# Kernel optimization log

Measured on AMD Instinct MI355X. Metric: run time of the kernel, lower is better.

Reference implementation:

```python
import jax, jax.numpy as jnp
import numpy as np

DIM_INPUT = 100000
DIM_LATENT = 128
NNZ = 819200
BATCH = 16384


def setup_inputs() -> dict:
    key = jax.random.key(0)
    k1, k2, k3, k4, k5 = jax.random.split(key, 5)
    vals = jax.random.uniform(k1, (NNZ,), dtype=jnp.float32)
    row_idx = jnp.sort(jax.random.randint(k2, (NNZ,), 0, BATCH, dtype=jnp.int32))
    col_idx = jax.random.randint(k3, (NNZ,), 0, DIM_INPUT, dtype=jnp.int32)
    # learned parameters (match torch init: w0 zeros, w/v randn)
    w0 = jnp.zeros((1,), dtype=jnp.float32)
    w = jax.random.normal(k4, (DIM_INPUT,), dtype=jnp.float32)
    v = jax.random.normal(k5, (DIM_INPUT, DIM_LATENT), dtype=jnp.float32)
    return {"vals": vals, "row_idx": row_idx, "col_idx": col_idx,
            "batch": BATCH, "w0": w0, "w": w, "v": v}


def reference(vals, row_idx, col_idx, batch, w0, w, v):
    # x is a sparse [batch, dim_input] matrix in COO form (row_idx, col_idx, vals).
    # linear term: w0 + x @ w
    linear = w0[0] + jax.ops.segment_sum(vals * w[col_idx], row_idx,
                                         num_segments=batch)
    # gather latent rows once: [nnz, K]
    v_rows = v[col_idx]
    weighted = vals[:, None] * v_rows                      # [nnz, K]
    xv = jax.ops.segment_sum(weighted, row_idx, num_segments=batch)       # [B, K]
    x_v_sq = jax.ops.segment_sum(weighted * v_rows, row_idx,
                                 num_segments=batch)       # x @ (v**2): [B, K]
    interaction = 0.5 * (jnp.sum(xv * xv, axis=1) - jnp.sum(x_v_sq, axis=1))
    return linear + interaction
```

## Files before the change

### kernel.cpp

```cpp
#include <hip/hip_runtime.h>

#define FM_NNZ   819200
#define FM_BATCH 16384
#define FM_DIM   100000
#define FM_K     128
#define NB_SHIFT 13
#define NBUCK    13
#define BAD_COL  (1 << 20)


static __device__ __forceinline__ uint32_t f2bf(float f) {
    uint32_t u = __float_as_uint(f);
    return (u + 0x7fffu + ((u >> 16) & 1u)) >> 16;
}

__global__ __launch_bounds__(256) void cvt_kernel(const float* __restrict__ v,
                                                  uint32_t* __restrict__ vb) {
    const float4* __restrict__ v4 = (const float4*)v;
    uint2* __restrict__ o = (uint2*)vb;
    const int n = (FM_DIM * FM_K) / 4;
    for (int i = blockIdx.x * blockDim.x + threadIdx.x; i < n;
         i += gridDim.x * blockDim.x) {
        const float4 x = v4[i];
        uint2 r;
        r.x = f2bf(x.x) | (f2bf(x.y) << 16);
        r.y = f2bf(x.z) | (f2bf(x.w) << 16);
        o[i] = r;
    }
}


__global__ __launch_bounds__(256, 8) void fm_fwd_kernel(
    const float* __restrict__ vals,
    const int*   __restrict__ row_idx,
    const int*   __restrict__ col_idx,
    const float* __restrict__ w0,
    const float* __restrict__ w_,
    const uint32_t* __restrict__ vb,
    float*       __restrict__ out)
{
    const int wave = threadIdx.x >> 6;
    const int lane = threadIdx.x & 63;
    const int wid  = blockIdx.x * 4 + wave;
    const int row0 = 2 * wid;
    const int row1 = row0 + 1;

    int s[3];
    #pragma unroll
    for (int q = 0; q < 3; ++q) {
        const int key = row0 + q;
        int lo = 0, hi = FM_NNZ;
        while (lo < hi) {
            const int mid = (lo + hi) >> 1;
            if (row_idx[mid] < key) lo = mid + 1; else hi = mid;
        }
        s[q] = lo;
    }
    const int s0 = s[0], s1 = s[1], s2 = s[2];

    int   cA, cB, cC, cD;
    float aA, aB, aC, aD;
    {
        int idx, ic; bool ok;
        idx = s0 + lane;      ok = idx < s1; ic = min(idx, FM_NNZ - 1);
        cA = ok ? col_idx[ic] : BAD_COL;  aA = ok ? vals[ic] : 0.f;
        idx = s0 + 64 + lane; ok = idx < s1; ic = min(idx, FM_NNZ - 1);
        cB = ok ? col_idx[ic] : BAD_COL;  aB = ok ? vals[ic] : 0.f;
        idx = s1 + lane;      ok = idx < s2; ic = min(idx, FM_NNZ - 1);
        cC = ok ? col_idx[ic] : BAD_COL;  aC = ok ? vals[ic] : 0.f;
        idx = s1 + 64 + lane; ok = idx < s2; ic = min(idx, FM_NNZ - 1);
        cD = ok ? col_idx[ic] : BAD_COL;  aD = ok ? vals[ic] : 0.f;
    }

    float xv0l = 0.f, xv0h = 0.f, sq0l = 0.f, sq0h = 0.f, lin0 = 0.f;
    float xv1l = 0.f, xv1h = 0.f, sq1l = 0.f, sq1h = 0.f, lin1 = 0.f;

#define WALK(creg, areg, xlo, xhi, slo, shi, linr)                         \
    {                                                                      \
        unsigned long long m = __ballot(((creg) >> NB_SHIFT) == p);        \
        while (m) {                                                        \
            const int j = __ffsll((unsigned long long)m) - 1;              \
            m &= m - 1;                                                    \
            const int   cj = __shfl((creg), j);                            \
            const float aj = __shfl((areg), j);                            \
            const uint32_t u = vb[(size_t)cj * 64 + lane];                 \
            linr = fmaf(aj, w_[cj], linr);             \
            const float vlo = __uint_as_float(u << 16);                    \
            const float vhi = __uint_as_float(u & 0xffff0000u);            \
            const float tl = aj * vlo, th = aj * vhi;                      \
            xlo += tl;  xhi += th;                                         \
            slo = fmaf(tl, vlo, slo);  shi = fmaf(th, vhi, shi);           \
        }                                                                  \
    }

    for (int p = 0; p < NBUCK; ++p) {
        WALK(cA, aA, xv0l, xv0h, sq0l, sq0h, lin0)
        WALK(cB, aB, xv0l, xv0h, sq0l, sq0h, lin0)
        WALK(cC, aC, xv1l, xv1h, sq1l, sq1h, lin1)
        WALK(cD, aD, xv1l, xv1h, sq1l, sq1h, lin1)
    }
#undef WALK

    float part0 = xv0l * xv0l + xv0h * xv0h - sq0l - sq0h;
    float part1 = xv1l * xv1l + xv1h * xv1h - sq1l - sq1h;
    #pragma unroll
    for (int off = 32; off > 0; off >>= 1) {
        part0 += __shfl_down(part0, off);
        part1 += __shfl_down(part1, off);
    }
    if (lane == 0) {
        const float bias = w0[0];
        out[row0] = bias + lin0 + 0.5f * part0;
        out[row1] = bias + lin1 + 0.5f * part1;
    }
}

extern "C" void kernel_launch(void* const* d_in, const int* in_sizes, int n_in,
                              void* d_out, int out_size, void* d_ws, size_t ws_size,
                              hipStream_t stream) {
    const float* vals    = (const float*)d_in[0];
    const int*   row_idx = (const int*)  d_in[1];
    const int*   col_idx = (const int*)  d_in[2];
    const float* w0      = (const float*)d_in[4];
    const float* w       = (const float*)d_in[5];
    const float* v       = (const float*)d_in[6];
    float*       out     = (float*)d_out;
    uint32_t*    vb      = (uint32_t*)d_ws;

    cvt_kernel<<<1024, 256, 0, stream>>>(v, vb);
    fm_fwd_kernel<<<FM_BATCH / 8, 256, 0, stream>>>(
        vals, row_idx, col_idx, w0, w, vb, out);
}
```

Before: 174.7 us.

## Compact bucket-sorted nonzeros into LDS and batch gathers eight at a time

```diff
diff --git a/kernel.cpp b/kernel.cpp
--- a/kernel.cpp
+++ b/kernel.cpp
@@ -6,7 +6,7 @@
 #define FM_K     128
 #define NB_SHIFT 13
 #define NBUCK    13
-#define BAD_COL  (1 << 20)
+#define GBATCH   8
 
 
 static __device__ __forceinline__ uint32_t f2bf(float f) {
@@ -39,11 +39,12 @@
     const uint32_t* __restrict__ vb,
     float*       __restrict__ out)
 {
+    __shared__ uint2 lists[4][2][128];
+
     const int wave = threadIdx.x >> 6;
     const int lane = threadIdx.x & 63;
     const int wid  = blockIdx.x * 4 + wave;
     const int row0 = 2 * wid;
-    const int row1 = row0 + 1;
 
     int s[3];
     #pragma unroll
@@ -58,48 +59,84 @@
     }
     const int s0 = s[0], s1 = s[1], s2 = s[2];
 
-    int   cA, cB, cC, cD;
-    float aA, aB, aC, aD;
+    int cA, cB, cC, cD;  float aA, aB, aC, aD;  int bA, bB, bC, bD;
     {
         int idx, ic; bool ok;
         idx = s0 + lane;      ok = idx < s1; ic = min(idx, FM_NNZ - 1);
-        cA = ok ? col_idx[ic] : BAD_COL;  aA = ok ? vals[ic] : 0.f;
+        cA = col_idx[ic]; aA = ok ? vals[ic] : 0.f; bA = ok ? (cA >> NB_SHIFT) : 127;
         idx = s0 + 64 + lane; ok = idx < s1; ic = min(idx, FM_NNZ - 1);
-        cB = ok ? col_idx[ic] : BAD_COL;  aB = ok ? vals[ic] : 0.f;
+        cB = col_idx[ic]; aB = ok ? vals[ic] : 0.f; bB = ok ? (cB >> NB_SHIFT) : 127;
         idx = s1 + lane;      ok = idx < s2; ic = min(idx, FM_NNZ - 1);
-        cC = ok ? col_idx[ic] : BAD_COL;  aC = ok ? vals[ic] : 0.f;
+        cC = col_idx[ic]; aC = ok ? vals[ic] : 0.f; bC = ok ? (cC >> NB_SHIFT) : 127;
         idx = s1 + 64 + lane; ok = idx < s2; ic = min(idx, FM_NNZ - 1);
-        cD = ok ? col_idx[ic] : BAD_COL;  aD = ok ? vals[ic] : 0.f;
+        cD = col_idx[ic]; aD = ok ? vals[ic] : 0.f; bD = ok ? (cD >> NB_SHIFT) : 127;
     }
 
-    float xv0l = 0.f, xv0h = 0.f, sq0l = 0.f, sq0h = 0.f, lin0 = 0.f;
-    float xv1l = 0.f, xv1h = 0.f, sq1l = 0.f, sq1h = 0.f, lin1 = 0.f;
+    float lin0 = aA * w_[cA] + aB * w_[cB];
+    float lin1 = aC * w_[cC] + aD * w_[cD];
 
-#define WALK(creg, areg, xlo, xhi, slo, shi, linr)                         \
-    {                                                                      \
-        unsigned long long m = __ballot(((creg) >> NB_SHIFT) == p);        \
-        while (m) {                                                        \
-            const int j = __ffsll((unsigned long long)m) - 1;              \
-            m &= m - 1;                                                    \
-            const int   cj = __shfl((creg), j);                            \
-            const float aj = __shfl((areg), j);                            \
-            const uint32_t u = vb[(size_t)cj * 64 + lane];                 \
-            linr = fmaf(aj, w_[cj], linr);             \
-            const float vlo = __uint_as_float(u << 16);                    \
-            const float vhi = __uint_as_float(u & 0xffff0000u);            \
-            const float tl = aj * vlo, th = aj * vhi;                      \
-            xlo += tl;  xhi += th;                                         \
-            slo = fmaf(tl, vlo, slo);  shi = fmaf(th, vhi, shi);           \
-        }                                                                  \
+    const unsigned long long lt = (1ull << lane) - 1ull;
+    int total0, total1;
+    {
+        int posA = -1, posB = -1, run = 0;
+        for (int p = 0; p < NBUCK; ++p) {
+            const unsigned long long mA = __ballot(bA == p);
+            const unsigned long long mB = __ballot(bB == p);
+            const int nA = __popcll(mA);
+            if (bA == p) posA = run + __popcll(mA & lt);
+            if (bB == p) posB = run + nA + __popcll(mB & lt);
+            run += nA + __popcll(mB);
+        }
+        total0 = run;
+        if (posA >= 0) lists[wave][0][posA] = make_uint2((uint32_t)cA, __float_as_uint(aA));
+        if (posB >= 0) lists[wave][0][posB] = make_uint2((uint32_t)cB, __float_as_uint(aB));
+    }
+    {
+        int posC = -1, posD = -1, run = 0;
+        for (int p = 0; p < NBUCK; ++p) {
+            const unsigned long long mC = __ballot(bC == p);
+            const unsigned long long mD = __ballot(bD == p);
+            const int nC = __popcll(mC);
+            if (bC == p) posC = run + __popcll(mC & lt);
+            if (bD == p) posD = run + nC + __popcll(mD & lt);
+            run += nC + __popcll(mD);
+        }
+        total1 = run;
+        if (posC >= 0) lists[wave][1][posC] = make_uint2((uint32_t)cC, __float_as_uint(aC));
+        if (posD >= 0) lists[wave][1][posD] = make_uint2((uint32_t)cD, __float_as_uint(aD));
+    }
+    __syncthreads();
+
+    float xv0l = 0.f, xv0h = 0.f, sq0l = 0.f, sq0h = 0.f;
+    float xv1l = 0.f, xv1h = 0.f, sq1l = 0.f, sq1h = 0.f;
+
+#define ROWWALK(r, total, xvl, xvh, sql, sqh)                                 \
+    for (int i = 0; i < (total); i += GBATCH) {                               \
+        uint2    ca[GBATCH];                                                  \
+        uint32_t vv[GBATCH];                                                  \
+        _Pragma("unroll")                                                     \
+        for (int u = 0; u < GBATCH; ++u) {                                    \
+            const int e = min(i + u, (total) - 1);                            \
+            ca[u] = lists[wave][r][e];             \
+        }                                                                     \
+        _Pragma("unroll")                                                     \
+        for (int u = 0; u < GBATCH; ++u) {                                    \
+            vv[u] = vb[(size_t)ca[u].x * 64 + lane];  \
+        }                                                                     \
+        _Pragma("unroll")                                                     \
+        for (int u = 0; u < GBATCH; ++u) {                                    \
+            const float aj  = (i + u < (total)) ? __uint_as_float(ca[u].y) : 0.f; \
+            const float vlo = __uint_as_float(vv[u] << 16);                   \
+            const float vhi = __uint_as_float(vv[u] & 0xffff0000u);           \
+            const float tl = aj * vlo, th = aj * vhi;                         \
+            xvl += tl;  xvh += th;                                            \
+            sql = fmaf(tl, vlo, sql);  sqh = fmaf(th, vhi, sqh);              \
+        }                                                                     \
     }
 
-    for (int p = 0; p < NBUCK; ++p) {
-        WALK(cA, aA, xv0l, xv0h, sq0l, sq0h, lin0)
-        WALK(cB, aB, xv0l, xv0h, sq0l, sq0h, lin0)
-        WALK(cC, aC, xv1l, xv1h, sq1l, sq1h, lin1)
-        WALK(cD, aD, xv1l, xv1h, sq1l, sq1h, lin1)
-    }
-#undef WALK
+    ROWWALK(0, total0, xv0l, xv0h, sq0l, sq0h)
+    ROWWALK(1, total1, xv1l, xv1h, sq1l, sq1h)
+#undef ROWWALK
 
     float part0 = xv0l * xv0l + xv0h * xv0h - sq0l - sq0h;
     float part1 = xv1l * xv1l + xv1h * xv1h - sq1l - sq1h;
@@ -107,11 +144,13 @@
     for (int off = 32; off > 0; off >>= 1) {
         part0 += __shfl_down(part0, off);
         part1 += __shfl_down(part1, off);
+        lin0  += __shfl_down(lin0,  off);
+        lin1  += __shfl_down(lin1,  off);
     }
     if (lane == 0) {
         const float bias = w0[0];
-        out[row0] = bias + lin0 + 0.5f * part0;
-        out[row1] = bias + lin1 + 0.5f * part1;
+        out[row0]     = bias + lin0 + 0.5f * part0;
+        out[row0 + 1] = bias + lin1 + 0.5f * part1;
     }
 }
 
```

Result: faster. 149.8 us (-14.2%).
